# Performance work log

Measured on AMD Instinct MI355X. Metric: run time of the kernel, lower is better.

Reference implementation:

```python
import jax, jax.numpy as jnp
import numpy as np
from jax import lax

TAU = 20.0
DT = 1.0
V_TH = 1.0
V_RESET = 0.0


def lif_spike(x):
    # Heaviside spike (surrogate gradient only matters for backward)
    return (x > 0).astype(x.dtype)


def setup_inputs() -> dict:
    key = jax.random.key(0)
    k1, k2, k3 = jax.random.split(key, 3)
    T, B, IN, OUT = 100, 256, 1024, 1024
    input_spikes = jax.random.uniform(k1, (T, B, IN), dtype=jnp.float32)
    # nn.Linear default init: U(-1/sqrt(in), 1/sqrt(in)) scale; randn*0.03 is fine for a numeric baseline
    W = jax.random.normal(k2, (OUT, IN), dtype=jnp.float32) * (1.0 / np.sqrt(IN))
    b = jax.random.normal(k3, (OUT,), dtype=jnp.float32) * 0.01
    return {"input_spikes": input_spikes, "W": W, "b": b}


def reference(input_spikes, W, b):
    T, B, _ = input_spikes.shape
    OUT = W.shape[0]
    # Precompute all input currents with one big GEMM: [T,B,out]
    I_all = jnp.einsum('tbi,oi->tbo', input_spikes, W) + b

    def step(v, I):
        v = v + (-v / TAU + I) * DT          # leaky integration
        s = lif_spike(v - V_TH)              # threshold
        v = jnp.where(s > 0, V_RESET, v)     # reset on spike
        return v, s

    v0 = jnp.zeros((B, OUT), dtype=input_spikes.dtype)
    _, spikes = lax.scan(step, v0, I_all)
    return spikes  # [T, B, out]
```

## Files before the change

kernel.cpp:

```cpp
#include <hip/hip_runtime.h>


constexpr int kT   = 100;
constexpr int kB   = 256;
constexpr int kIn  = 1024;
constexpr int kOut = 1024;
constexpr int kM   = kT * kB;

constexpr int BM = 128;
constexpr int BN = 128;
constexpr int BK = 32;

__global__ __launch_bounds__(256, 3)
void gemm_f32(const float* __restrict__ A,
              const float* __restrict__ W,
              const float* __restrict__ bias,
              float* __restrict__ I)
{
    __shared__ float As[BK * BM];
    __shared__ float Ws[BK * BN];

    const int tid = threadIdx.x;
    const int m0  = blockIdx.y * BM;
    const int n0  = blockIdx.x * BN;

    const int tc = tid & 15;
    const int tr = tid >> 4;

    const int pw0 = (((2 * tc    ) ^ ((2 * tc    ) >> 2)) & 31) * 4;
    const int pw1 = (((2 * tc + 1) ^ ((2 * tc + 1) >> 2)) & 31) * 4;

    const int sr  = tid >> 1;
    const int sc0 = (tid & 1) * 16;
    const int wslot = ((((sr >> 2) ^ (sr >> 4)) & 31) * 4) + (sr & 3);

    const float* Arow = A + (size_t)(m0 + sr) * kIn + sc0;
    const float* Wrow = W + (size_t)(n0 + sr) * kIn + sc0;

    float4 la[4], lw[4];
#pragma unroll
    for (int i = 0; i < 4; ++i) {
        la[i] = *reinterpret_cast<const float4*>(Arow + i * 4);
        lw[i] = *reinterpret_cast<const float4*>(Wrow + i * 4);
    }

    float acc[8][8];
#pragma unroll
    for (int j = 0; j < 8; ++j)
#pragma unroll
        for (int l = 0; l < 8; ++l) acc[j][l] = 0.0f;

    for (int k0 = 0; k0 < kIn; k0 += BK) {
        __syncthreads();

#pragma unroll
        for (int i = 0; i < 4; ++i) {
            const float* lap = reinterpret_cast<const float*>(&la[i]);
            const float* lwp = reinterpret_cast<const float*>(&lw[i]);
#pragma unroll
            for (int kk = 0; kk < 4; ++kk) {
                const int k = sc0 + i * 4 + kk;
                As[k * BM + sr]    = lap[kk];
                Ws[k * BN + wslot] = lwp[kk];
            }
        }

        __syncthreads();

        if (k0 + BK < kIn) {
            const int kn = k0 + BK;
#pragma unroll
            for (int i = 0; i < 4; ++i) {
                la[i] = *reinterpret_cast<const float4*>(Arow + kn + i * 4);
                lw[i] = *reinterpret_cast<const float4*>(Wrow + kn + i * 4);
            }
        }

#pragma unroll 2
        for (int k = 0; k < BK; ++k) {
            const float4 a0 = *reinterpret_cast<const float4*>(&As[k * BM + tr * 8]);
            const float4 a1 = *reinterpret_cast<const float4*>(&As[k * BM + tr * 8 + 4]);
            const float4 w0 = *reinterpret_cast<const float4*>(&Ws[k * BN + pw0]);
            const float4 w1 = *reinterpret_cast<const float4*>(&Ws[k * BN + pw1]);
            const float a[8] = {a0.x, a0.y, a0.z, a0.w, a1.x, a1.y, a1.z, a1.w};
            const float w[8] = {w0.x, w0.y, w0.z, w0.w, w1.x, w1.y, w1.z, w1.w};
#pragma unroll
            for (int j = 0; j < 8; ++j)
#pragma unroll
                for (int l = 0; l < 8; ++l)
                    acc[j][l] = fmaf(a[j], w[l], acc[j][l]);
        }
    }

#pragma unroll
    for (int j = 0; j < 8; ++j) {
        const int m = m0 + tr * 8 + j;
#pragma unroll
        for (int h = 0; h < 2; ++h) {
            const int n = n0 + tc * 8 + h * 4;
            float4 o4;
            o4.x = acc[j][h * 4 + 0] + bias[n + 0];
            o4.y = acc[j][h * 4 + 1] + bias[n + 1];
            o4.z = acc[j][h * 4 + 2] + bias[n + 2];
            o4.w = acc[j][h * 4 + 3] + bias[n + 3];
            *reinterpret_cast<float4*>(&I[(size_t)m * kOut + n]) = o4;
        }
    }
}

__global__ __launch_bounds__(256)
void lif_scan_f32(const float* Iin, float* out)
{
    const int idx4 = (blockIdx.x * blockDim.x + threadIdx.x) * 4;
    if (idx4 >= kB * kOut) return;

    float v0 = 0.0f, v1 = 0.0f, v2 = 0.0f, v3 = 0.0f;
    for (int t = 0; t < kT; ++t) {
        const size_t off = (size_t)t * (kB * kOut) + idx4;
        const float4 Iv = *reinterpret_cast<const float4*>(&Iin[off]);
        float4 s4;

        { const float t1 = v0 / 20.0f; const float u = Iv.x - t1; v0 = v0 + u;
          const bool s = (v0 > 1.0f); s4.x = s ? 1.0f : 0.0f; if (s) v0 = 0.0f; }
        { const float t1 = v1 / 20.0f; const float u = Iv.y - t1; v1 = v1 + u;
          const bool s = (v1 > 1.0f); s4.y = s ? 1.0f : 0.0f; if (s) v1 = 0.0f; }
        { const float t1 = v2 / 20.0f; const float u = Iv.z - t1; v2 = v2 + u;
          const bool s = (v2 > 1.0f); s4.z = s ? 1.0f : 0.0f; if (s) v2 = 0.0f; }
        { const float t1 = v3 / 20.0f; const float u = Iv.w - t1; v3 = v3 + u;
          const bool s = (v3 > 1.0f); s4.w = s ? 1.0f : 0.0f; if (s) v3 = 0.0f; }

        *reinterpret_cast<float4*>(&out[off]) = s4;
    }
}

extern "C" void kernel_launch(void* const* d_in, const int* in_sizes, int n_in,
                              void* d_out, int out_size, void* d_ws, size_t ws_size,
                              hipStream_t stream) {
    const float* spikes = (const float*)d_in[0];
    const float* W      = (const float*)d_in[1];
    const float* bias   = (const float*)d_in[2];
    float* out = (float*)d_out;

    const size_t iBytes = (size_t)kM * kOut * sizeof(float);
    dim3 grid(kOut / BN, kM / BM);

    float* Ibuf = (ws_size >= iBytes && d_ws != nullptr) ? (float*)d_ws : out;
    gemm_f32<<<grid, 256, 0, stream>>>(spikes, W, bias, Ibuf);
    lif_scan_f32<<<(kB * kOut) / (256 * 4), 256, 0, stream>>>(Ibuf, out);
}
```

Baseline: 678.9 us.

## Double-buffer GEMM shared-memory tiles with BK=16 and drop one barrier

Switches the FP32 GEMM to ping-pong shared-memory buffers so each k-tile is written to the other buffer. That lets the leading __syncthreads per iteration go away, leaving one barrier per tile. BK is halved to 16 to keep LDS usage the same, occupancy is raised to 4 blocks per CU, and the inner-loop unroll goes from 2 to 4. In exchange there are twice as many k-iterations and barriers overall, and fewer staging registers per thread.

```diff
diff --git a/kernel.cpp b/kernel.cpp
--- a/kernel.cpp
+++ b/kernel.cpp
@@ -9,16 +9,17 @@
 
 constexpr int BM = 128;
 constexpr int BN = 128;
-constexpr int BK = 32;
+constexpr int BK = 16;
+constexpr int NT = kIn / BK;
 
-__global__ __launch_bounds__(256, 3)
+__global__ __launch_bounds__(256, 4)
 void gemm_f32(const float* __restrict__ A,
               const float* __restrict__ W,
               const float* __restrict__ bias,
               float* __restrict__ I)
 {
-    __shared__ float As[BK * BM];
-    __shared__ float Ws[BK * BN];
+    __shared__ float As[2][BK * BM];
+    __shared__ float Ws[2][BK * BN];
 
     const int tid = threadIdx.x;
     const int m0  = blockIdx.y * BM;
@@ -31,15 +32,14 @@
     const int pw1 = (((2 * tc + 1) ^ ((2 * tc + 1) >> 2)) & 31) * 4;
 
     const int sr  = tid >> 1;
-    const int sc0 = (tid & 1) * 16;
+    const int sc0 = (tid & 1) * 8;
+    const float* Arow = A + (size_t)(m0 + sr) * kIn + sc0;
+    const float* Wrow = W + (size_t)(n0 + sr) * kIn + sc0;
     const int wslot = ((((sr >> 2) ^ (sr >> 4)) & 31) * 4) + (sr & 3);
 
-    const float* Arow = A + (size_t)(m0 + sr) * kIn + sc0;
-    const float* Wrow = W + (size_t)(n0 + sr) * kIn + sc0;
-
-    float4 la[4], lw[4];
+    float4 la[2], lw[2];
 #pragma unroll
-    for (int i = 0; i < 4; ++i) {
+    for (int i = 0; i < 2; ++i) {
         la[i] = *reinterpret_cast<const float4*>(Arow + i * 4);
         lw[i] = *reinterpret_cast<const float4*>(Wrow + i * 4);
     }
@@ -50,38 +50,39 @@
 #pragma unroll
         for (int l = 0; l < 8; ++l) acc[j][l] = 0.0f;
 
-    for (int k0 = 0; k0 < kIn; k0 += BK) {
-        __syncthreads();
+    for (int t = 0; t < NT; ++t) {
+        float* Ab = As[t & 1];
+        float* Wb = Ws[t & 1];
 
 #pragma unroll
-        for (int i = 0; i < 4; ++i) {
-            const float* lap = reinterpret_cast<const float*>(&la[i]);
-            const float* lwp = reinterpret_cast<const float*>(&lw[i]);
+        for (int i = 0; i < 2; ++i) {
+            const float* pa = reinterpret_cast<const float*>(&la[i]);
+            const float* pw = reinterpret_cast<const float*>(&lw[i]);
 #pragma unroll
             for (int kk = 0; kk < 4; ++kk) {
                 const int k = sc0 + i * 4 + kk;
-                As[k * BM + sr]    = lap[kk];
-                Ws[k * BN + wslot] = lwp[kk];
+                Ab[k * BM + sr]    = pa[kk];
+                Wb[k * BN + wslot] = pw[kk];
             }
         }
 
         __syncthreads();
 
-        if (k0 + BK < kIn) {
-            const int kn = k0 + BK;
+        if (t + 1 < NT) {
+            const int kn = (t + 1) * BK;
 #pragma unroll
-            for (int i = 0; i < 4; ++i) {
+            for (int i = 0; i < 2; ++i) {
                 la[i] = *reinterpret_cast<const float4*>(Arow + kn + i * 4);
                 lw[i] = *reinterpret_cast<const float4*>(Wrow + kn + i * 4);
             }
         }
 
-#pragma unroll 2
+#pragma unroll 4
         for (int k = 0; k < BK; ++k) {
-            const float4 a0 = *reinterpret_cast<const float4*>(&As[k * BM + tr * 8]);
-            const float4 a1 = *reinterpret_cast<const float4*>(&As[k * BM + tr * 8 + 4]);
-            const float4 w0 = *reinterpret_cast<const float4*>(&Ws[k * BN + pw0]);
-            const float4 w1 = *reinterpret_cast<const float4*>(&Ws[k * BN + pw1]);
+            const float4 a0 = *reinterpret_cast<const float4*>(&Ab[k * BM + tr * 8]);
+            const float4 a1 = *reinterpret_cast<const float4*>(&Ab[k * BM + tr * 8 + 4]);
+            const float4 w0 = *reinterpret_cast<const float4*>(&Wb[k * BN + pw0]);
+            const float4 w1 = *reinterpret_cast<const float4*>(&Wb[k * BN + pw1]);
             const float a[8] = {a0.x, a0.y, a0.z, a0.w, a1.x, a1.y, a1.z, a1.w};
             const float w[8] = {w0.x, w0.y, w0.z, w0.w, w1.x, w1.y, w1.z, w1.w};
 #pragma unroll
```

Result: no change. 672.2 us (-1.0%).
